# Optimization experiments

Measured on AMD Instinct MI355X. Metric: run time of the kernel, lower is better.

Reference implementation:

```python
import jax, jax.numpy as jnp
import numpy as np

B, H0, D = 8192, 64, 32
HIDDEN = [128, 128, 128]


def setup_inputs() -> dict:
    key = jax.random.key(0)
    ks = jax.random.split(key, 4)
    x = jax.random.normal(ks[0], (B, H0, D), dtype=jnp.float32)
    # he_normal: std = sqrt(2 / fan_in), fan_in ~= h_i * h0 for a [h_{i+1}, h_i, h0] kernel
    hs = [H0] + HIDDEN
    kernels = []
    for i in range(len(HIDDEN)):
        fan_in = hs[i] * hs[0]
        std = np.sqrt(2.0 / fan_in).astype(np.float32)
        kernels.append(jax.random.normal(ks[i + 1], (hs[i + 1], hs[i], hs[0]), dtype=jnp.float32) * std)
    return {
        'x': x,
        'k0': kernels[0], 'k1': kernels[1], 'k2': kernels[2],
        'b0': jnp.zeros((HIDDEN[0],), jnp.float32),
        'b1': jnp.zeros((HIDDEN[1],), jnp.float32),
        'b2': jnp.zeros((HIDDEN[2],), jnp.float32),
    }


def _cin(x, kernels, biases):
    # x: (b, h0, d). Layer i: feature_map[b,k,d] = relu( sum_{g,h} x_i[b,g,d] * x_0[b,h,d] * K[k,g,h] + bias[k] )
    x0 = x
    xi = x
    pooled = []
    for K, bias in zip(kernels, biases):
        fm = jnp.einsum('bgd,bhd,kgh->bkd', xi, x0, K) + bias[None, :, None]
        fm = jax.nn.relu(fm)
        xi = fm
        pooled.append(jnp.sum(fm, axis=-1))  # (b, hk)
    return jnp.concatenate(pooled, axis=-1)  # (b, sum(hidden))


def reference(x, k0, k1, k2, b0, b1, b2):
    return _cin(x, (k0, k1, k2), (b0, b1, b2))
```

## Files before the change

kernel.cpp:

```cpp
#include <hip/hip_runtime.h>

typedef unsigned short ushort_t;
typedef unsigned int u32;
typedef __attribute__((ext_vector_type(8))) short bf16x8;
typedef __attribute__((ext_vector_type(4))) float f32x4;
typedef __attribute__((ext_vector_type(2))) float f32x2;
typedef __attribute__((ext_vector_type(4))) u32 u32x4;

#define NTOT 262144

__device__ __forceinline__ ushort_t f2b_rne(float f) {
    u32 u = __builtin_bit_cast(u32, f);
    u32 r = u + 0x7FFFu + ((u >> 16) & 1u);
    return (ushort_t)(r >> 16);
}
__device__ __forceinline__ u32 scale_pack(f32x2 xp, f32x2 s) {
    f32x2 d;
    asm("v_pk_mul_f32 %0, %1, %2" : "=v"(d) : "v"(xp), "v"(s));
    u32 r;
    asm("v_cvt_pk_bf16_f32 %0, %1, %2" : "=v"(r) : "v"(d[0]), "v"(d[1]));
    return r;
}
__device__ __forceinline__ void gl_lds16(const ushort_t* g, ushort_t* l) {
    __builtin_amdgcn_global_load_lds(
        (const __attribute__((address_space(1))) u32*)g,
        (__attribute__((address_space(3))) u32*)l, 16, 0, 0);
}

__global__ void cin_prep_x0bf(const float* __restrict__ x, ushort_t* __restrict__ x0bf) {
    __shared__ float xs[64 * 33];
    const int b = blockIdx.x, t = threadIdx.x;
    const float4* src = (const float4*)(x + (size_t)b * 2048);
#pragma unroll
    for (int i = 0; i < 2; ++i) {
        float4 f = src[t + 256 * i];
        int e = (t + 256 * i) * 4;
        int h = e >> 5, d = e & 31;
        xs[h * 33 + d]     = f.x;
        xs[h * 33 + d + 1] = f.y;
        xs[h * 33 + d + 2] = f.z;
        xs[h * 33 + d + 3] = f.w;
    }
    __syncthreads();
    const int d = t >> 3, j8 = t & 7;
    u32 w[4];
#pragma unroll
    for (int q = 0; q < 4; ++q) {
        int h0 = j8 * 8 + 2 * q;
        w[q] = (u32)f2b_rne(xs[h0 * 33 + d]) | ((u32)f2b_rne(xs[(h0 + 1) * 33 + d]) << 16);
    }
    uint4 o; o.x = w[0]; o.y = w[1]; o.z = w[2]; o.w = w[3];
    *(uint4*)(x0bf + ((size_t)b * 32 + d) * 64 + j8 * 8) = o;
}

__global__ void cin_prep_k2(const float* __restrict__ K, ushort_t* __restrict__ Kp, int G) {
    const int g = blockIdx.x, t = threadIdx.x;
    const int k = t >> 1, j0 = (t & 1) * 16;
    const float* s = K + ((size_t)k * G + g) * 64 + j0 * 2;
    u32* dst = (u32*)(Kp + (size_t)g * 8192 + k * 64);
    const int swc = k & 7;
#pragma unroll
    for (int c = 0; c < 4; ++c) {
        u32 w[4];
#pragma unroll
        for (int q = 0; q < 4; ++q) {
            int e = (c * 4 + q) * 2;
            w[q] = (u32)f2b_rne(s[e]) | ((u32)f2b_rne(s[e + 1]) << 16);
        }
        uint4 o; o.x = w[0]; o.y = w[1]; o.z = w[2]; o.w = w[3];
        *(uint4*)(dst + (((j0 >> 2) + c) ^ swc) * 4) = o;
    }
}

template <int G, bool STORE_FM>
__launch_bounds__(256, 2)
__global__ void cin_layer5(const ushort_t* __restrict__ x0bf,
                           const ushort_t* __restrict__ xi_src,
                           const ushort_t* __restrict__ Kp,
                           const float* __restrict__ bias,
                           ushort_t* __restrict__ fm_out,
                           float* __restrict__ out,
                           int layer_off) {
    constexpr int NC = G / 8;
    __shared__ ushort_t k_lds[3 * 8192];

    const int t = threadIdx.x;
    const int wg = blockIdx.x;
    const int lane = t & 63;
    const int wave = t >> 6;
    const int wm = wave >> 1, wn = wave & 1;
    const int col = lane & 15, g4 = lane >> 4;
    const int swz = (col & 7) << 3;
    const size_t n0 = (size_t)wg * 128;

    auto issueK = [&](int kg, int slot) {
        const ushort_t* src = Kp + (size_t)kg * 8192 + (size_t)t * 8;
        ushort_t* dst = k_lds + slot * 8192 + t * 8;
#pragma unroll
        for (int i = 0; i < 4; ++i) gl_lds16(src + i * 2048, dst + i * 2048);
    };

    const ushort_t* xrow[4];
#pragma unroll
    for (int nf = 0; nf < 4; ++nf)
        xrow[nf] = xi_src + (n0 + wn * 64 + nf * 16 + col) * G;

    f32x2 xb[4][8];
#pragma unroll
    for (int nf = 0; nf < 4; ++nf) {
        const size_t n_g = n0 + wn * 64 + nf * 16 + col;
#pragma unroll
        for (int ks2 = 0; ks2 < 2; ++ks2) {
            u32x4 v = *(const u32x4*)(x0bf + n_g * 64 + ks2 * 32 + g4 * 8);
#pragma unroll
            for (int q = 0; q < 4; ++q) {
                f32x2 p;
                p[0] = __builtin_bit_cast(float, v[q] << 16);
                p[1] = __builtin_bit_cast(float, v[q] & 0xFFFF0000u);
                xb[nf][ks2 * 4 + q] = p;
            }
        }
    }

    u32x4 xcA[4], xcB[4];
#pragma unroll
    for (int nf = 0; nf < 4; ++nf) xcA[nf] = *(const u32x4*)(xrow[nf]);

    issueK(0, 0);
    issueK(1, 1);

    f32x4 acc[4][4];
#pragma unroll
    for (int a = 0; a < 4; ++a)
#pragma unroll
        for (int b = 0; b < 4; ++b) acc[a][b] = (f32x4){0.f, 0.f, 0.f, 0.f};

    asm volatile("s_waitcnt vmcnt(4)" ::: "memory");
    __builtin_amdgcn_s_barrier();
    __builtin_amdgcn_sched_barrier(0);

    int sr = 0, sw = 2;

    auto CHUNK = [&](int c, u32x4 (&cur)[4], u32x4 (&nxt)[4]) {
#pragma unroll
        for (int gi = 0; gi < 8; ++gi) {
            const int g = c * 8 + gi;
            if (gi == 0) {
                int cn = c + 1; if (cn > NC - 1) cn = NC - 1;
#pragma unroll
                for (int nf = 0; nf < 4; ++nf)
                    nxt[nf] = *(const u32x4*)(xrow[nf] + cn * 8);
            }
            int kg = g + 2; if (kg > G - 1) kg = G - 1;
            issueK(kg, sw);
            bf16x8 bw[4][2];
#pragma unroll
            for (int nf = 0; nf < 4; ++nf) {
                u32 xw = cur[nf][gi >> 1];
                u32 xs32 = (gi & 1) ? (xw & 0xFFFF0000u) : (xw << 16);
                float xf = __builtin_bit_cast(float, xs32);
                f32x2 s; s[0] = xf; s[1] = xf;
#pragma unroll
                for (int ks2 = 0; ks2 < 2; ++ks2) {
                    u32x4 o;
#pragma unroll
                    for (int q = 0; q < 4; ++q)
                        o[q] = scale_pack(xb[nf][ks2 * 4 + q], s);
                    bw[nf][ks2] = __builtin_bit_cast(bf16x8, o);
                }
            }
            const ushort_t* kbuf = k_lds + sr * 8192;
#pragma unroll
            for (int ks2 = 0; ks2 < 2; ++ks2) {
                bf16x8 af[4];
#pragma unroll
                for (int mf = 0; mf < 4; ++mf)
                    af[mf] = *(const bf16x8*)(kbuf + (wm * 64 + mf * 16 + col) * 64 +
                                              ((ks2 * 32 + g4 * 8) ^ swz));
                __builtin_amdgcn_s_setprio(1);
#pragma unroll
                for (int mf = 0; mf < 4; ++mf)
#pragma unroll
                    for (int nf = 0; nf < 4; ++nf)
                        acc[mf][nf] = __builtin_amdgcn_mfma_f32_16x16x32_bf16(
                            af[mf], bw[nf][ks2], acc[mf][nf], 0, 0, 0);
                __builtin_amdgcn_s_setprio(0);
            }
            asm volatile("s_waitcnt vmcnt(4)" ::: "memory");
            __builtin_amdgcn_s_barrier();
            __builtin_amdgcn_sched_barrier(0);
            sr = (sr == 2) ? 0 : sr + 1;
            sw = (sw == 2) ? 0 : sw + 1;
        }
    };

#pragma unroll 1
    for (int c = 0; c < NC; c += 2) {
        CHUNK(c, xcA, xcB);
        CHUNK(c + 1, xcB, xcA);
    }

#pragma unroll
    for (int mf = 0; mf < 4; ++mf) {
        const int kk = wm * 64 + mf * 16 + g4 * 4;
        const float4 bs = *(const float4*)(bias + kk);
        float pool[2][4] = {{0.f, 0.f, 0.f, 0.f}, {0.f, 0.f, 0.f, 0.f}};
#pragma unroll
        for (int nf = 0; nf < 4; ++nf) {
            const size_t n_g = n0 + wn * 64 + nf * 16 + col;
            float v[4];
#pragma unroll
            for (int r = 0; r < 4; ++r) {
                float vv = acc[mf][nf][r] + ((r == 0) ? bs.x : (r == 1) ? bs.y : (r == 2) ? bs.z : bs.w);
                vv = fmaxf(vv, 0.f);
                v[r] = vv;
                pool[nf >> 1][r] += vv;
            }
            if (STORE_FM) {
                uint2 ww;
                ww.x = (u32)f2b_rne(v[0]) | ((u32)f2b_rne(v[1]) << 16);
                ww.y = (u32)f2b_rne(v[2]) | ((u32)f2b_rne(v[3]) << 16);
                *(uint2*)(fm_out + n_g * 128 + kk) = ww;
            }
        }
#pragma unroll
        for (int bi = 0; bi < 2; ++bi) {
#pragma unroll
            for (int r = 0; r < 4; ++r) {
                float s = pool[bi][r];
                s += __shfl_xor(s, 1, 16);
                s += __shfl_xor(s, 2, 16);
                s += __shfl_xor(s, 4, 16);
                s += __shfl_xor(s, 8, 16);
                pool[bi][r] = s;
            }
            if (col == 0) {
                const long b = (long)wg * 4 + wn * 2 + bi;
                float4 o;
                o.x = pool[bi][0]; o.y = pool[bi][1]; o.z = pool[bi][2]; o.w = pool[bi][3];
                *(float4*)(out + b * 384 + layer_off + kk) = o;
            }
        }
    }
}

extern "C" void kernel_launch(void* const* d_in, const int* in_sizes, int n_in,
                              void* d_out, int out_size, void* d_ws, size_t ws_size,
                              hipStream_t stream) {
    const float* x  = (const float*)d_in[0];
    const float* k0 = (const float*)d_in[1];
    const float* k1 = (const float*)d_in[2];
    const float* k2 = (const float*)d_in[3];
    const float* bb0 = (const float*)d_in[4];
    const float* bb1 = (const float*)d_in[5];
    const float* bb2 = (const float*)d_in[6];
    float* out = (float*)d_out;
    char* ws = (char*)d_ws;

    ushort_t* x0bf = (ushort_t*)(ws);
    ushort_t* Kp0  = (ushort_t*)(ws + 33554432);
    ushort_t* Kp1  = (ushort_t*)(ws + 34603008);
    ushort_t* Kp2  = (ushort_t*)(ws + 36700160);
    ushort_t* fm0  = (ushort_t*)(ws + 38797312);
    ushort_t* fm1  = (ushort_t*)(ws + 105906176);

    cin_prep_x0bf<<<8192, 256, 0, stream>>>(x, x0bf);
    cin_prep_k2<<<64, 256, 0, stream>>>(k0, Kp0, 64);
    cin_prep_k2<<<128, 256, 0, stream>>>(k1, Kp1, 128);
    cin_prep_k2<<<128, 256, 0, stream>>>(k2, Kp2, 128);

    cin_layer5<64, true><<<2048, 256, 0, stream>>>(x0bf, x0bf, Kp0, bb0, fm0, out, 0);
    cin_layer5<128, true><<<2048, 256, 0, stream>>>(x0bf, fm0, Kp1, bb1, fm1, out, 128);
    cin_layer5<128, false><<<2048, 256, 0, stream>>>(x0bf, fm1, Kp2, bb2, (ushort_t*)nullptr, out, 256);
}
```

Measured before the change: 1.268 ms.

## Load K slices in pairs with double buffering, halving barriers per layer

The K staging pipeline changes from a triple-buffered ring of single g-slices (prefetch depth 2, one barrier per slice) to a double buffer of g-slice pairs, with one barrier per pair. The aim is to cut barrier and waitcnt overhead per MFMA block. In exchange, prefetch depth drops to one pair and each iteration waits on vmcnt(0), so global-to-LDS latency may be less well hidden. LDS use rises from 48KB to 64KB per block, which may affect occupancy at two blocks per CU.

```diff
diff --git a/kernel.cpp b/kernel.cpp
--- a/kernel.cpp
+++ b/kernel.cpp
@@ -74,15 +74,16 @@
 
 template <int G, bool STORE_FM>
 __launch_bounds__(256, 2)
-__global__ void cin_layer5(const ushort_t* __restrict__ x0bf,
+__global__ void cin_layer6(const ushort_t* __restrict__ x0bf,
                            const ushort_t* __restrict__ xi_src,
                            const ushort_t* __restrict__ Kp,
                            const float* __restrict__ bias,
                            ushort_t* __restrict__ fm_out,
                            float* __restrict__ out,
                            int layer_off) {
-    constexpr int NC = G / 8;
-    __shared__ ushort_t k_lds[3 * 8192];
+    constexpr int NIT = G / 2;
+    constexpr int NBODY = G / 8;
+    __shared__ ushort_t k_lds[2][16384];
 
     const int t = threadIdx.x;
     const int wg = blockIdx.x;
@@ -93,11 +94,11 @@
     const int swz = (col & 7) << 3;
     const size_t n0 = (size_t)wg * 128;
 
-    auto issueK = [&](int kg, int slot) {
-        const ushort_t* src = Kp + (size_t)kg * 8192 + (size_t)t * 8;
-        ushort_t* dst = k_lds + slot * 8192 + t * 8;
-#pragma unroll
-        for (int i = 0; i < 4; ++i) gl_lds16(src + i * 2048, dst + i * 2048);
+    auto issuePair = [&](int p, int buf) {
+        const ushort_t* src = Kp + (size_t)p * 16384 + (size_t)t * 8;
+        ushort_t* dst = &k_lds[buf][0] + t * 8;
+#pragma unroll
+        for (int i = 0; i < 8; ++i) gl_lds16(src + i * 2048, dst + i * 2048);
     };
 
     const ushort_t* xrow[4];
@@ -126,8 +127,7 @@
 #pragma unroll
     for (int nf = 0; nf < 4; ++nf) xcA[nf] = *(const u32x4*)(xrow[nf]);
 
-    issueK(0, 0);
-    issueK(1, 1);
+    issuePair(0, 0);
 
     f32x4 acc[4][4];
 #pragma unroll
@@ -135,29 +135,21 @@
 #pragma unroll
         for (int b = 0; b < 4; ++b) acc[a][b] = (f32x4){0.f, 0.f, 0.f, 0.f};
 
-    asm volatile("s_waitcnt vmcnt(4)" ::: "memory");
+    asm volatile("s_waitcnt vmcnt(0)" ::: "memory");
     __builtin_amdgcn_s_barrier();
     __builtin_amdgcn_sched_barrier(0);
 
-    int sr = 0, sw = 2;
-
-    auto CHUNK = [&](int c, u32x4 (&cur)[4], u32x4 (&nxt)[4]) {
-#pragma unroll
-        for (int gi = 0; gi < 8; ++gi) {
-            const int g = c * 8 + gi;
-            if (gi == 0) {
-                int cn = c + 1; if (cn > NC - 1) cn = NC - 1;
-#pragma unroll
-                for (int nf = 0; nf < 4; ++nf)
-                    nxt[nf] = *(const u32x4*)(xrow[nf] + cn * 8);
-            }
-            int kg = g + 2; if (kg > G - 1) kg = G - 1;
-            issueK(kg, sw);
+    auto ITER = [&](int it, int bufr , const u32x4 (&cur)[4], int j ) {
+        int pn = it + 1; if (pn > NIT - 1) pn = NIT - 1;
+        issuePair(pn, bufr ^ 1);
+        const ushort_t* kbuf = &k_lds[bufr][0];
+#pragma unroll
+        for (int sub = 0; sub < 2; ++sub) {
             bf16x8 bw[4][2];
 #pragma unroll
             for (int nf = 0; nf < 4; ++nf) {
-                u32 xw = cur[nf][gi >> 1];
-                u32 xs32 = (gi & 1) ? (xw & 0xFFFF0000u) : (xw << 16);
+                u32 xw = cur[nf][j];
+                u32 xs32 = sub ? (xw & 0xFFFF0000u) : (xw << 16);
                 float xf = __builtin_bit_cast(float, xs32);
                 f32x2 s; s[0] = xf; s[1] = xf;
 #pragma unroll
@@ -169,13 +161,13 @@
                     bw[nf][ks2] = __builtin_bit_cast(bf16x8, o);
                 }
             }
-            const ushort_t* kbuf = k_lds + sr * 8192;
 #pragma unroll
             for (int ks2 = 0; ks2 < 2; ++ks2) {
                 bf16x8 af[4];
 #pragma unroll
                 for (int mf = 0; mf < 4; ++mf)
-                    af[mf] = *(const bf16x8*)(kbuf + (wm * 64 + mf * 16 + col) * 64 +
+                    af[mf] = *(const bf16x8*)(kbuf + sub * 8192 +
+                                              (wm * 64 + mf * 16 + col) * 64 +
                                               ((ks2 * 32 + g4 * 8) ^ swz));
                 __builtin_amdgcn_s_setprio(1);
 #pragma unroll
@@ -186,18 +178,34 @@
                             af[mf], bw[nf][ks2], acc[mf][nf], 0, 0, 0);
                 __builtin_amdgcn_s_setprio(0);
             }
-            asm volatile("s_waitcnt vmcnt(4)" ::: "memory");
-            __builtin_amdgcn_s_barrier();
-            __builtin_amdgcn_sched_barrier(0);
-            sr = (sr == 2) ? 0 : sr + 1;
-            sw = (sw == 2) ? 0 : sw + 1;
-        }
+        }
+        asm volatile("s_waitcnt vmcnt(0)" ::: "memory");
+        __builtin_amdgcn_s_barrier();
+        __builtin_amdgcn_sched_barrier(0);
     };
 
 #pragma unroll 1
-    for (int c = 0; c < NC; c += 2) {
-        CHUNK(c, xcA, xcB);
-        CHUNK(c + 1, xcB, xcA);
+    for (int bp = 0; bp < NBODY / 2; ++bp) {
+        {
+            int cn = 2 * bp + 1; if (cn > NBODY - 1) cn = NBODY - 1;
+#pragma unroll
+            for (int nf = 0; nf < 4; ++nf) xcB[nf] = *(const u32x4*)(xrow[nf] + cn * 8);
+            const int itB = bp * 8;
+            ITER(itB + 0, 0, xcA, 0);
+            ITER(itB + 1, 1, xcA, 1);
+            ITER(itB + 2, 0, xcA, 2);
+            ITER(itB + 3, 1, xcA, 3);
+        }
+        {
+            int cn = 2 * bp + 2; if (cn > NBODY - 1) cn = NBODY - 1;
+#pragma unroll
+            for (int nf = 0; nf < 4; ++nf) xcA[nf] = *(const u32x4*)(xrow[nf] + cn * 8);
+            const int itB = bp * 8 + 4;
+            ITER(itB + 0, 0, xcB, 0);
+            ITER(itB + 1, 1, xcB, 1);
+            ITER(itB + 2, 0, xcB, 2);
+            ITER(itB + 3, 1, xcB, 3);
+        }
     }
 
 #pragma unroll
@@ -269,7 +277,7 @@
     cin_prep_k2<<<128, 256, 0, stream>>>(k1, Kp1, 128);
     cin_prep_k2<<<128, 256, 0, stream>>>(k2, Kp2, 128);
 
-    cin_layer5<64, true><<<2048, 256, 0, stream>>>(x0bf, x0bf, Kp0, bb0, fm0, out, 0);
-    cin_layer5<128, true><<<2048, 256, 0, stream>>>(x0bf, fm0, Kp1, bb1, fm1, out, 128);
-    cin_layer5<128, false><<<2048, 256, 0, stream>>>(x0bf, fm1, Kp2, bb2, (ushort_t*)nullptr, out, 256);
-}
+    cin_layer6<64, true><<<2048, 256, 0, stream>>>(x0bf, x0bf, Kp0, bb0, fm0, out, 0);
+    cin_layer6<128, true><<<2048, 256, 0, stream>>>(x0bf, fm0, Kp1, bb1, fm1, out, 128);
+    cin_layer6<128, false><<<2048, 256, 0, stream>>>(x0bf, fm1, Kp2, bb2, (ushort_t*)nullptr, out, 256);
+}
```

Result: no change. 1.288 ms (+1.6%).

## Load kernel fragments directly from global memory instead of LDS triple buffering

Applied to the files above, without the earlier changes.

Drops the LDS triple-buffered async staging of the per-g weight slice and the per-g barriers. Each wave now reads its K fragments straight from global memory, relying on L1/L2 since every workgroup reuses the same small weight tensor. The weight prep drops the XOR swizzle to match plain row-major reads, and synchronisation is reduced to one __syncthreads per chunk of 8 g. The cost is that global-load latency is no longer hidden by explicit prefetch, so MFMA issue may stall on those loads.

```diff
diff --git a/kernel.cpp b/kernel.cpp
--- a/kernel.cpp
+++ b/kernel.cpp
@@ -20,11 +20,6 @@
     u32 r;
     asm("v_cvt_pk_bf16_f32 %0, %1, %2" : "=v"(r) : "v"(d[0]), "v"(d[1]));
     return r;
-}
-__device__ __forceinline__ void gl_lds16(const ushort_t* g, ushort_t* l) {
-    __builtin_amdgcn_global_load_lds(
-        (const __attribute__((address_space(1))) u32*)g,
-        (__attribute__((address_space(3))) u32*)l, 16, 0, 0);
 }
 
 __global__ void cin_prep_x0bf(const float* __restrict__ x, ushort_t* __restrict__ x0bf) {
@@ -53,28 +48,27 @@
     *(uint4*)(x0bf + ((size_t)b * 32 + d) * 64 + j8 * 8) = o;
 }
 
-__global__ void cin_prep_k2(const float* __restrict__ K, ushort_t* __restrict__ Kp, int G) {
+__global__ void cin_prep_k3(const float* __restrict__ K, ushort_t* __restrict__ Kp, int G) {
     const int g = blockIdx.x, t = threadIdx.x;
-    const int k = t >> 1, j0 = (t & 1) * 16;
-    const float* s = K + ((size_t)k * G + g) * 64 + j0 * 2;
-    u32* dst = (u32*)(Kp + (size_t)g * 8192 + k * 64);
-    const int swc = k & 7;
+    const int k = t >> 1, j0 = (t & 1) * 32;
+    const float* s = K + ((size_t)k * G + g) * 64 + j0;
+    ushort_t* dst = Kp + (size_t)g * 8192 + k * 64 + j0;
 #pragma unroll
     for (int c = 0; c < 4; ++c) {
         u32 w[4];
 #pragma unroll
         for (int q = 0; q < 4; ++q) {
-            int e = (c * 4 + q) * 2;
+            int e = c * 8 + 2 * q;
             w[q] = (u32)f2b_rne(s[e]) | ((u32)f2b_rne(s[e + 1]) << 16);
         }
         uint4 o; o.x = w[0]; o.y = w[1]; o.z = w[2]; o.w = w[3];
-        *(uint4*)(dst + (((j0 >> 2) + c) ^ swc) * 4) = o;
+        *(uint4*)(dst + c * 8) = o;
     }
 }
 
 template <int G, bool STORE_FM>
 __launch_bounds__(256, 2)
-__global__ void cin_layer5(const ushort_t* __restrict__ x0bf,
+__global__ void cin_layer7(const ushort_t* __restrict__ x0bf,
                            const ushort_t* __restrict__ xi_src,
                            const ushort_t* __restrict__ Kp,
                            const float* __restrict__ bias,
@@ -82,7 +76,6 @@
                            float* __restrict__ out,
                            int layer_off) {
     constexpr int NC = G / 8;
-    __shared__ ushort_t k_lds[3 * 8192];
 
     const int t = threadIdx.x;
     const int wg = blockIdx.x;
@@ -90,20 +83,14 @@
     const int wave = t >> 6;
     const int wm = wave >> 1, wn = wave & 1;
     const int col = lane & 15, g4 = lane >> 4;
-    const int swz = (col & 7) << 3;
     const size_t n0 = (size_t)wg * 128;
-
-    auto issueK = [&](int kg, int slot) {
-        const ushort_t* src = Kp + (size_t)kg * 8192 + (size_t)t * 8;
-        ushort_t* dst = k_lds + slot * 8192 + t * 8;
-#pragma unroll
-        for (int i = 0; i < 4; ++i) gl_lds16(src + i * 2048, dst + i * 2048);
-    };
 
     const ushort_t* xrow[4];
 #pragma unroll
     for (int nf = 0; nf < 4; ++nf)
         xrow[nf] = xi_src + (n0 + wn * 64 + nf * 16 + col) * G;
+
+    const ushort_t* kbase = Kp + (size_t)(wm * 64 + col) * 64 + g4 * 8;
 
     f32x2 xb[4][8];
 #pragma unroll
@@ -126,72 +113,57 @@
 #pragma unroll
     for (int nf = 0; nf < 4; ++nf) xcA[nf] = *(const u32x4*)(xrow[nf]);
 
-    issueK(0, 0);
-    issueK(1, 1);
-
     f32x4 acc[4][4];
 #pragma unroll
     for (int a = 0; a < 4; ++a)
 #pragma unroll
         for (int b = 0; b < 4; ++b) acc[a][b] = (f32x4){0.f, 0.f, 0.f, 0.f};
 
-    asm volatile("s_waitcnt vmcnt(4)" ::: "memory");
-    __builtin_amdgcn_s_barrier();
-    __builtin_amdgcn_sched_barrier(0);
-
-    int sr = 0, sw = 2;
-
-    auto CHUNK = [&](int c, u32x4 (&cur)[4], u32x4 (&nxt)[4]) {
-#pragma unroll
-        for (int gi = 0; gi < 8; ++gi) {
-            const int g = c * 8 + gi;
-            if (gi == 0) {
-                int cn = c + 1; if (cn > NC - 1) cn = NC - 1;
+    auto PROC_G = [&](int g, const u32x4 (&cur)[4], int j, int sub) {
+        const ushort_t* kg = kbase + (size_t)g * 8192;
+        bf16x8 af[2][4];
+#pragma unroll
+        for (int ks2 = 0; ks2 < 2; ++ks2)
+#pragma unroll
+            for (int mf = 0; mf < 4; ++mf)
+                af[ks2][mf] = *(const bf16x8*)(kg + mf * 1024 + ks2 * 32);
+        bf16x8 bw[2][4];
+#pragma unroll
+        for (int nf = 0; nf < 4; ++nf) {
+            u32 xw = cur[nf][j];
+            u32 xs32 = sub ? (xw & 0xFFFF0000u) : (xw << 16);
+            float xf = __builtin_bit_cast(float, xs32);
+            f32x2 s; s[0] = xf; s[1] = xf;
+#pragma unroll
+            for (int ks2 = 0; ks2 < 2; ++ks2) {
+                u32x4 o;
+#pragma unroll
+                for (int q = 0; q < 4; ++q)
+                    o[q] = scale_pack(xb[nf][ks2 * 4 + q], s);
+                bw[ks2][nf] = __builtin_bit_cast(bf16x8, o);
+            }
+        }
+#pragma unroll
+        for (int ks2 = 0; ks2 < 2; ++ks2) {
+            __builtin_amdgcn_s_setprio(1);
+#pragma unroll
+            for (int mf = 0; mf < 4; ++mf)
 #pragma unroll
                 for (int nf = 0; nf < 4; ++nf)
-                    nxt[nf] = *(const u32x4*)(xrow[nf] + cn * 8);
-            }
-            int kg = g + 2; if (kg > G - 1) kg = G - 1;
-            issueK(kg, sw);
-            bf16x8 bw[4][2];
-#pragma unroll
-            for (int nf = 0; nf < 4; ++nf) {
-                u32 xw = cur[nf][gi >> 1];
-                u32 xs32 = (gi & 1) ? (xw & 0xFFFF0000u) : (xw << 16);
-                float xf = __builtin_bit_cast(float, xs32);
-                f32x2 s; s[0] = xf; s[1] = xf;
-#pragma unroll
-                for (int ks2 = 0; ks2 < 2; ++ks2) {
-                    u32x4 o;
-#pragma unroll
-                    for (int q = 0; q < 4; ++q)
-                        o[q] = scale_pack(xb[nf][ks2 * 4 + q], s);
-                    bw[nf][ks2] = __builtin_bit_cast(bf16x8, o);
-                }
-            }
-            const ushort_t* kbuf = k_lds + sr * 8192;
-#pragma unroll
-            for (int ks2 = 0; ks2 < 2; ++ks2) {
-                bf16x8 af[4];
-#pragma unroll
-                for (int mf = 0; mf < 4; ++mf)
-                    af[mf] = *(const bf16x8*)(kbuf + (wm * 64 + mf * 16 + col) * 64 +
-                                              ((ks2 * 32 + g4 * 8) ^ swz));
-                __builtin_amdgcn_s_setprio(1);
-#pragma unroll
-                for (int mf = 0; mf < 4; ++mf)
-#pragma unroll
-                    for (int nf = 0; nf < 4; ++nf)
-                        acc[mf][nf] = __builtin_amdgcn_mfma_f32_16x16x32_bf16(
-                            af[mf], bw[nf][ks2], acc[mf][nf], 0, 0, 0);
-                __builtin_amdgcn_s_setprio(0);
-            }
-            asm volatile("s_waitcnt vmcnt(4)" ::: "memory");
-            __builtin_amdgcn_s_barrier();
-            __builtin_amdgcn_sched_barrier(0);
-            sr = (sr == 2) ? 0 : sr + 1;
-            sw = (sw == 2) ? 0 : sw + 1;
-        }
+                    acc[mf][nf] = __builtin_amdgcn_mfma_f32_16x16x32_bf16(
+                        af[ks2][mf], bw[ks2][nf], acc[mf][nf], 0, 0, 0);
+            __builtin_amdgcn_s_setprio(0);
+        }
+    };
+
+    auto CHUNK = [&](int c, const u32x4 (&cur)[4], u32x4 (&nxt)[4]) {
+        int cn = c + 1; if (cn > NC - 1) cn = NC - 1;
+#pragma unroll
+        for (int nf = 0; nf < 4; ++nf) nxt[nf] = *(const u32x4*)(xrow[nf] + cn * 8);
+#pragma unroll
+        for (int gi = 0; gi < 8; ++gi)
+            PROC_G(c * 8 + gi, cur, gi >> 1, gi & 1);
+        __syncthreads();
     };
 
 #pragma unroll 1
@@ -265,11 +237,11 @@
     ushort_t* fm1  = (ushort_t*)(ws + 105906176);
 
     cin_prep_x0bf<<<8192, 256, 0, stream>>>(x, x0bf);
-    cin_prep_k2<<<64, 256, 0, stream>>>(k0, Kp0, 64);
-    cin_prep_k2<<<128, 256, 0, stream>>>(k1, Kp1, 128);
-    cin_prep_k2<<<128, 256, 0, stream>>>(k2, Kp2, 128);
-
-    cin_layer5<64, true><<<2048, 256, 0, stream>>>(x0bf, x0bf, Kp0, bb0, fm0, out, 0);
-    cin_layer5<128, true><<<2048, 256, 0, stream>>>(x0bf, fm0, Kp1, bb1, fm1, out, 128);
-    cin_layer5<128, false><<<2048, 256, 0, stream>>>(x0bf, fm1, Kp2, bb2, (ushort_t*)nullptr, out, 256);
-}
+    cin_prep_k3<<<64, 256, 0, stream>>>(k0, Kp0, 64);
+    cin_prep_k3<<<128, 256, 0, stream>>>(k1, Kp1, 128);
+    cin_prep_k3<<<128, 256, 0, stream>>>(k2, Kp2, 128);
+
+    cin_layer7<64, true><<<2048, 256, 0, stream>>>(x0bf, x0bf, Kp0, bb0, fm0, out, 0);
+    cin_layer7<128, true><<<2048, 256, 0, stream>>>(x0bf, fm0, Kp1, bb1, fm1, out, 128);
+    cin_layer7<128, false><<<2048, 256, 0, stream>>>(x0bf, fm1, Kp2, bb2, (ushort_t*)nullptr, out, 256);
+}
```

Result: slower. 2.447 ms (+93.0%).
